# Optimization experiments

Measured on AMD Instinct MI355X. Metric: run time of the kernel, lower is better.

Reference implementation:

```python
import jax, jax.numpy as jnp
import numpy as np

NEG_SLOPE = 0.2


def gat_conv(x, src, dst, N, W, a_src, a_dst, b, concat):
    # x: [N, F_in], W: [F_in, H*C], a_src/a_dst: [H, C], b: [H*C] or [C]
    H, C = a_src.shape
    h = (x @ W).reshape(N, H, C)                    # [N, H, C]
    al_src = jnp.einsum('nhc,hc->nh', h, a_src)     # [N, H]
    al_dst = jnp.einsum('nhc,hc->nh', h, a_dst)     # [N, H]
    logits = jax.nn.leaky_relu(al_src[src] + al_dst[dst], NEG_SLOPE)  # [E, H]
    # edge softmax over incoming edges of each destination node
    m = jax.ops.segment_max(logits, dst, num_segments=N)              # [N, H]
    m = jnp.where(jnp.isfinite(m), m, 0.0)
    e = jnp.exp(logits - m[dst])                                      # [E, H]
    denom = jax.ops.segment_sum(e, dst, num_segments=N)               # [N, H]
    alpha = e / denom[dst]                                            # [E, H]
    out = jax.ops.segment_sum(alpha[:, :, None] * h[src], dst, num_segments=N)  # [N, H, C]
    if concat:
        return out.reshape(N, H * C) + b
    return out.mean(axis=1) + b


def setup_inputs() -> dict:
    key = jax.random.key(0)
    ks = jax.random.split(key, 12)
    N, E = 100000, 1600000
    F_in, Ch, Co, H = 128, 32, 64, 4
    x = jax.random.normal(ks[0], (N, F_in), dtype=jnp.float32)
    edge_index = jax.random.randint(ks[1], (2, E), 0, N, dtype=jnp.int64)
    s = 0.1
    return {
        'x': x, 'edge_index': edge_index,
        'W1': jax.random.normal(ks[2], (F_in, H * Ch), jnp.float32) * s,
        'a_src1': jax.random.normal(ks[3], (H, Ch), jnp.float32) * s,
        'a_dst1': jax.random.normal(ks[4], (H, Ch), jnp.float32) * s,
        'b1': jnp.zeros((H * Ch,), jnp.float32),
        'W2': jax.random.normal(ks[5], (H * Ch, H * Ch), jnp.float32) * s,
        'a_src2': jax.random.normal(ks[6], (H, Ch), jnp.float32) * s,
        'a_dst2': jax.random.normal(ks[7], (H, Ch), jnp.float32) * s,
        'b2': jnp.zeros((H * Ch,), jnp.float32),
        'W3': jax.random.normal(ks[8], (H * Ch, H * Co), jnp.float32) * s,
        'a_src3': jax.random.normal(ks[9], (H, Co), jnp.float32) * s,
        'a_dst3': jax.random.normal(ks[10], (H, Co), jnp.float32) * s,
        'b3': jnp.zeros((Co,), jnp.float32),
    }


def reference(x, edge_index, W1, a_src1, a_dst1, b1, W2, a_src2, a_dst2, b2, W3, a_src3, a_dst3, b3):
    N = x.shape[0]
    # PyG GATConv default add_self_loops=True
    loop = jnp.arange(N, dtype=edge_index.dtype)
    src = jnp.concatenate([edge_index[0], loop])
    dst = jnp.concatenate([edge_index[1], loop])
    h = gat_conv(x, src, dst, N, W1, a_src1, a_dst1, b1, concat=True)
    h = jax.nn.elu(h)
    h = gat_conv(h, src, dst, N, W2, a_src2, a_dst2, b2, concat=True)
    h = jax.nn.elu(h)
    out = gat_conv(h, src, dst, N, W3, a_src3, a_dst3, b3, concat=False)
    return out
```

## Files before the change

kernel.cpp:

```cpp
#include <hip/hip_runtime.h>


#define NEG_SLOPE 0.2f

typedef __attribute__((ext_vector_type(8))) _Float16 half8v;
typedef __attribute__((ext_vector_type(4))) _Float16 half4v;
typedef __attribute__((ext_vector_type(2))) _Float16 half2v;
typedef __attribute__((ext_vector_type(4))) float f32x4;

__device__ __forceinline__ float lrelu(float v) { return v > 0.f ? v : NEG_SLOPE * v; }

struct hf2 { _Float16 hi, lo; };
__device__ __forceinline__ hf2 split_f16(float f)
{
    hf2 r;
    r.hi = (_Float16)f;
    r.lo = (_Float16)(f - (float)r.hi);
    return r;
}

__global__ void fill_sentinel(float* __restrict__ out, int n)
{
    int i = blockIdx.x * blockDim.x + threadIdx.x;
    if (i < n) out[i] = 1e30f;
}

__global__ void detect_idx64(const int* __restrict__ ei, int* __restrict__ flag)
{
    __shared__ int anynz;
    if (threadIdx.x == 0) anynz = 0;
    __syncthreads();
    int v = ei[2 * threadIdx.x + 1];
    if (v != 0) atomicOr(&anynz, 1);
    __syncthreads();
    if (threadIdx.x == 0) flag[0] = (anynz == 0) ? 1 : 0;
}

__global__ void prep_edges(const void* __restrict__ ei, const int* __restrict__ flag,
                           int* __restrict__ deg8, int* __restrict__ loc, int N, int E)
{
    int e = blockIdx.x * blockDim.x + threadIdx.x;
    if (e >= E) return;
    int xcc;
    asm("s_getreg_b32 %0, hwreg(HW_REG_XCC_ID)" : "=s"(xcc));
    xcc &= 7;
    int d;
    if (flag[0]) d = (int)__builtin_nontemporal_load((const long long*)ei + E + e);
    else         d = __builtin_nontemporal_load((const int*)ei + E + e);
    int v = atomicAdd(&deg8[xcc * N + d], 1);
    loc[e] = (xcc << 28) | v;
}

__global__ void reduce8(int* __restrict__ deg8, int* __restrict__ deg, int N)
{
    int d = blockIdx.x * blockDim.x + threadIdx.x;
    if (d >= N) return;
    int s = 0;
    #pragma unroll
    for (int k = 0; k < 8; ++k) {
        int v = deg8[k * N + d];
        deg8[k * N + d] = s;
        s += v;
    }
    deg[d] = s;
}

__global__ __launch_bounds__(256)
void scanA(const int* __restrict__ deg, int* __restrict__ rowptr,
           int* __restrict__ bsum, int N)
{
    __shared__ int part[256];
    const int t = threadIdx.x;
    const int base = blockIdx.x * 1024 + t * 4;
    int v[4];
    #pragma unroll
    for (int j = 0; j < 4; ++j) v[j] = (base + j < N) ? deg[base + j] : 0;
    int s = v[0] + v[1] + v[2] + v[3];
    part[t] = s;
    __syncthreads();
    #pragma unroll
    for (int off = 1; off < 256; off <<= 1) {
        int p = (t >= off) ? part[t - off] : 0;
        __syncthreads();
        part[t] += p;
        __syncthreads();
    }
    int run = (t == 0) ? 0 : part[t - 1];
    #pragma unroll
    for (int j = 0; j < 4; ++j) {
        if (base + j < N) rowptr[base + j] = run;
        run += v[j];
    }
    if (t == 255) bsum[blockIdx.x] = part[255];
}

__global__ __launch_bounds__(1024)
void scanB(int* __restrict__ bsum, int nb)
{
    __shared__ int s[1024];
    int t = threadIdx.x;
    s[t] = (t < nb) ? bsum[t] : 0;
    __syncthreads();
    for (int off = 1; off < 1024; off <<= 1) {
        int p = (t >= off) ? s[t - off] : 0;
        __syncthreads();
        s[t] += p;
        __syncthreads();
    }
    if (t < nb) bsum[t] = (t == 0) ? 0 : s[t - 1];
}

__global__ __launch_bounds__(256)
void scanC(int* __restrict__ rowptr, const int* __restrict__ bsum, int N, int E)
{
    const int base = blockIdx.x * 1024 + threadIdx.x * 4;
    const int off = bsum[blockIdx.x];
    #pragma unroll
    for (int j = 0; j < 4; ++j)
        if (base + j < N) rowptr[base + j] += off;
    if (blockIdx.x == 0 && threadIdx.x == 0) rowptr[N] = E;
}

__global__ void fill_csr(const void* __restrict__ ei, const int* __restrict__ flag,
                         const int* __restrict__ loc, const int* __restrict__ rowptr,
                         const int* __restrict__ deg8, int* __restrict__ csr_src,
                         int N, int E)
{
    int e = blockIdx.x * blockDim.x + threadIdx.x;
    if (e >= E) return;
    int s, d;
    if (flag[0]) {
        s = (int)__builtin_nontemporal_load((const long long*)ei + e);
        d = (int)__builtin_nontemporal_load((const long long*)ei + E + e);
    } else {
        s = __builtin_nontemporal_load((const int*)ei + e);
        d = __builtin_nontemporal_load((const int*)ei + E + e);
    }
    int lv = loc[e];
    csr_src[rowptr[d] + deg8[(lv >> 28) * N + d] + (lv & 0x0FFFFFFF)] = s;
}

__global__ __launch_bounds__(256)
void convert_wt(const float* __restrict__ W, _Float16* __restrict__ wthi,
                _Float16* __restrict__ wtlo, int ldw, int wcol0)
{
    int t = blockIdx.x * 256 + threadIdx.x;
    int k = t >> 7, n = t & 127;
    float v = W[(long long)k * ldw + wcol0 + n];
    hf2 r = split_f16(v);
    wthi[n * 128 + k] = r.hi;
    wtlo[n * 128 + k] = r.lo;
}

template<int HPC, bool AF32>
__global__ __launch_bounds__(256, 2)
void gemm_mfma(const void* __restrict__ Aptr, const _Float16* __restrict__ Alo,
               const _Float16* __restrict__ Wthi, const _Float16* __restrict__ Wtlo,
               _Float16* __restrict__ Chi, int ldc, int colofs, int hofs,
               const float* __restrict__ aS, const float* __restrict__ aD,
               float* __restrict__ als, float* __restrict__ ald, int M)
{
    const int tid = threadIdx.x;
    const int wave = tid >> 6, lane = tid & 63;
    const int l15 = lane & 15, lk = lane >> 4;
    const int m0 = blockIdx.x * 128 + wave * 32;

    f32x4 acc[2][8];
    #pragma unroll
    for (int rg = 0; rg < 2; ++rg)
        #pragma unroll
        for (int i = 0; i < 8; ++i) acc[rg][i] = (f32x4){0.f, 0.f, 0.f, 0.f};

    #pragma unroll
    for (int kt = 0; kt < 4; ++kt) {
        const int k = kt * 32 + lk * 8;
        half8v bh[8], bl[8];
        #pragma unroll
        for (int nf = 0; nf < 8; ++nf) {
            bh[nf] = *(const half8v*)&Wthi[(nf * 16 + l15) * 128 + k];
            bl[nf] = *(const half8v*)&Wtlo[(nf * 16 + l15) * 128 + k];
        }
        #pragma unroll
        for (int rg = 0; rg < 2; ++rg) {
            int mrow = m0 + rg * 16 + l15;
            if (mrow >= M) mrow = M - 1;
            half8v ah, al;
            if (AF32) {
                const float* A32 = (const float*)Aptr;
                float4 v0 = *(const float4*)&A32[(long long)mrow * 128 + k];
                float4 v1 = *(const float4*)&A32[(long long)mrow * 128 + k + 4];
                hf2 s0 = split_f16(v0.x), s1 = split_f16(v0.y), s2 = split_f16(v0.z), s3 = split_f16(v0.w);
                hf2 s4 = split_f16(v1.x), s5 = split_f16(v1.y), s6 = split_f16(v1.z), s7 = split_f16(v1.w);
                ah[0] = s0.hi; ah[1] = s1.hi; ah[2] = s2.hi; ah[3] = s3.hi;
                ah[4] = s4.hi; ah[5] = s5.hi; ah[6] = s6.hi; ah[7] = s7.hi;
                al[0] = s0.lo; al[1] = s1.lo; al[2] = s2.lo; al[3] = s3.lo;
                al[4] = s4.lo; al[5] = s5.lo; al[6] = s6.lo; al[7] = s7.lo;
            } else {
                const _Float16* Ahi = (const _Float16*)Aptr;
                ah = *(const half8v*)&Ahi[(long long)mrow * 128 + k];
                al = *(const half8v*)&Alo[(long long)mrow * 128 + k];
            }
            #pragma unroll
            for (int nf = 0; nf < 8; ++nf) {
                acc[rg][nf] = __builtin_amdgcn_mfma_f32_16x16x32_f16(ah, bh[nf], acc[rg][nf], 0, 0, 0);
                acc[rg][nf] = __builtin_amdgcn_mfma_f32_16x16x32_f16(ah, bl[nf], acc[rg][nf], 0, 0, 0);
                acc[rg][nf] = __builtin_amdgcn_mfma_f32_16x16x32_f16(al, bh[nf], acc[rg][nf], 0, 0, 0);
            }
        }
    }

    float asv[8], adv[8];
    #pragma unroll
    for (int nf = 0; nf < 8; ++nf) {
        asv[nf] = aS[nf * 16 + l15];
        adv[nf] = aD[nf * 16 + l15];
    }
    constexpr int NFH = 8 / HPC;

    #pragma unroll
    for (int rg = 0; rg < 2; ++rg) {
        #pragma unroll
        for (int r = 0; r < 4; ++r) {
            int gm = m0 + rg * 16 + lk * 4 + r;
            if (gm >= M) continue;
            #pragma unroll
            for (int nf = 0; nf < 8; ++nf)
                Chi[(long long)gm * ldc + colofs + nf * 16 + l15] = (_Float16)acc[rg][nf][r];
        }
        #pragma unroll
        for (int r = 0; r < 4; ++r) {
            #pragma unroll
            for (int h = 0; h < HPC; ++h) {
                float ps = 0.f, pd = 0.f;
                #pragma unroll
                for (int q = 0; q < NFH; ++q) {
                    int nf = h * NFH + q;
                    ps += acc[rg][nf][r] * asv[nf];
                    pd += acc[rg][nf][r] * adv[nf];
                }
                #pragma unroll
                for (int m = 1; m < 16; m <<= 1) {
                    ps += __shfl_xor(ps, m);
                    pd += __shfl_xor(pd, m);
                }
                if (l15 == 0) {
                    int gm = m0 + rg * 16 + lk * 4 + r;
                    if (gm < M) {
                        als[gm * 4 + hofs + h] = ps;
                        ald[gm * 4 + hofs + h] = pd;
                    }
                }
            }
        }
    }
}

template<int C, int HL>
__global__ __launch_bounds__(256)
void gat_aggregate(const int* __restrict__ rowptr, const int* __restrict__ csr_src,
                   const float* __restrict__ als, const float* __restrict__ ald,
                   const _Float16* __restrict__ h16, const float* __restrict__ bias,
                   _Float16* __restrict__ ohi, _Float16* __restrict__ olo, int N)
{
    constexpr int ROW = HL * C;
    constexpr int LOG2HL = (HL == 4) ? 2 : 1;
    const int d = (blockIdx.x * blockDim.x + threadIdx.x) >> 6;
    const int lane = threadIdx.x & 63;
    if (d >= N) return;
    const int j = lane * 2;
    const int hh = j / C;

    const int myh = lane & (HL - 1);
    const int myi = lane >> LOG2HL;
    const float ald_mine = ald[d * 4 + myh];

    const float wself = __expf(lrelu(als[d * 4 + hh] + ald[d * 4 + hh]));
    float denom = wself;
    half2v hv = *(const half2v*)&h16[(unsigned)d * ROW + j];
    float vx = wself * (float)hv.x, vy = wself * (float)hv.y;

    const int e0 = rowptr[d], e1 = rowptr[d + 1];
    for (int base = e0; base < e1; base += 8) {
        int sv_mine = 0;
        float w_mine = 0.f;
        if (lane < 8 * HL) {
            int ee = base + myi;
            sv_mine = csr_src[ee < e1 ? ee : e1 - 1];
            float a = als[sv_mine * 4 + myh] + ald_mine;
            w_mine = (ee < e1) ? __expf(lrelu(a)) : 0.f;
        }
        int sref[8];
        half2v hb[8];
        #pragma unroll
        for (int i = 0; i < 8; ++i) sref[i] = __shfl(sv_mine, i * HL, 64);
        #pragma unroll
        for (int i = 0; i < 8; ++i) hb[i] = *(const half2v*)&h16[(unsigned)sref[i] * ROW + j];
        #pragma unroll
        for (int i = 0; i < 8; ++i) {
            float wv = __shfl(w_mine, i * HL + hh, 64);
            denom += wv;
            vx += wv * (float)hb[i].x;
            vy += wv * (float)hb[i].y;
        }
    }
    float inv = 1.f / denom;
    vx = vx * inv + bias[j];
    vy = vy * inv + bias[j + 1];
    vx = vx > 0.f ? vx : __expf(vx) - 1.f;
    vy = vy > 0.f ? vy : __expf(vy) - 1.f;
    hf2 rx = split_f16(vx), ry = split_f16(vy);
    half2v hi2, lo2;
    hi2.x = rx.hi; hi2.y = ry.hi;
    lo2.x = rx.lo; lo2.y = ry.lo;
    *(half2v*)&ohi[(unsigned)d * ROW + j] = hi2;
    *(half2v*)&olo[(unsigned)d * ROW + j] = lo2;
}

__global__ __launch_bounds__(256)
void gat_aggregate3(const int* __restrict__ rowptr, const int* __restrict__ csr_src,
                    const float* __restrict__ als, const float* __restrict__ ald,
                    const _Float16* __restrict__ h16, const float* __restrict__ bias,
                    float* __restrict__ out, int N)
{
    const int d = (blockIdx.x * blockDim.x + threadIdx.x) >> 6;
    const int lane = threadIdx.x & 63;
    if (d >= N) return;
    const int q = lane * 4;
    const int chd = lane >> 4;

    const int myh = lane & 3;
    const int myi = lane >> 2;
    const float ald_mine = ald[d * 4 + myh];

    const float wself = __expf(lrelu(als[d * 4 + chd] + ald[d * 4 + chd]));
    float dn = wself;
    half4v hs = *(const half4v*)&h16[(unsigned)d * 256 + q];
    float vx0 = wself * (float)hs.x, vx1 = wself * (float)hs.y;
    float vx2 = wself * (float)hs.z, vx3 = wself * (float)hs.w;

    const int e0 = rowptr[d], e1 = rowptr[d + 1];
    for (int base = e0; base < e1; base += 8) {
        int sv_mine = 0;
        float w_mine = 0.f;
        if (lane < 32) {
            int ee = base + myi;
            sv_mine = csr_src[ee < e1 ? ee : e1 - 1];
            float a = als[sv_mine * 4 + myh] + ald_mine;
            w_mine = (ee < e1) ? __expf(lrelu(a)) : 0.f;
        }
        int sref[8];
        half4v hb[8];
        #pragma unroll
        for (int i = 0; i < 8; ++i) sref[i] = __shfl(sv_mine, i * 4, 64);
        #pragma unroll
        for (int i = 0; i < 8; ++i) hb[i] = *(const half4v*)&h16[(unsigned)sref[i] * 256 + q];
        #pragma unroll
        for (int i = 0; i < 8; ++i) {
            float wv = __shfl(w_mine, i * 4 + chd, 64);
            dn += wv;
            vx0 += wv * (float)hb[i].x;
            vx1 += wv * (float)hb[i].y;
            vx2 += wv * (float)hb[i].z;
            vx3 += wv * (float)hb[i].w;
        }
    }
    const float s = 0.25f / dn;
    float m0 = vx0 * s, m1 = vx1 * s, m2 = vx2 * s, m3 = vx3 * s;
    m0 += __shfl_xor(m0, 16); m1 += __shfl_xor(m1, 16);
    m2 += __shfl_xor(m2, 16); m3 += __shfl_xor(m3, 16);
    m0 += __shfl_xor(m0, 32); m1 += __shfl_xor(m1, 32);
    m2 += __shfl_xor(m2, 32); m3 += __shfl_xor(m3, 32);
    if (lane < 16) {
        m0 += bias[q + 0]; m1 += bias[q + 1];
        m2 += bias[q + 2]; m3 += bias[q + 3];
        *(float4*)&out[(unsigned)d * 64 + q] = make_float4(m0, m1, m2, m3);
    }
}

extern "C" void kernel_launch(void* const* d_in, const int* in_sizes, int n_in,
                              void* d_out, int out_size, void* d_ws, size_t ws_size,
                              hipStream_t stream)
{
    const float* x      = (const float*)d_in[0];
    const void*  ei     = d_in[1];
    const float* W1     = (const float*)d_in[2];
    const float* a_src1 = (const float*)d_in[3];
    const float* a_dst1 = (const float*)d_in[4];
    const float* b1     = (const float*)d_in[5];
    const float* W2     = (const float*)d_in[6];
    const float* a_src2 = (const float*)d_in[7];
    const float* a_dst2 = (const float*)d_in[8];
    const float* b2     = (const float*)d_in[9];
    const float* W3     = (const float*)d_in[10];
    const float* a_src3 = (const float*)d_in[11];
    const float* a_dst3 = (const float*)d_in[12];
    const float* b3     = (const float*)d_in[13];

    const int N = in_sizes[0] / 128;
    const int E = in_sizes[1] / 2;

    char* w = (char*)d_ws;
    auto alloc = [&](size_t bytes) {
        char* p = w;
        w += (bytes + 255) & ~(size_t)255;
        return p;
    };
    int*      flag    = (int*)     alloc(256);
    int*      deg8    = (int*)     alloc((size_t)N * 8 * 4);
    int*      deg     = (int*)     alloc((size_t)N * 4);
    int*      rowptr  = (int*)     alloc((size_t)(N + 1) * 4);
    int*      bsum    = (int*)     alloc(1024 * 4);
    int*      loc     = (int*)     alloc((size_t)E * 4);
    int*      csr_src = (int*)     alloc((size_t)E * 4);
    _Float16* hhi     = (_Float16*)alloc((size_t)N * 256 * 2);
    _Float16* xhi     = (_Float16*)alloc((size_t)N * 128 * 2);
    _Float16* xlo     = (_Float16*)alloc((size_t)N * 128 * 2);
    float*    als     = (float*)   alloc((size_t)N * 4 * 4);
    float*    ald     = (float*)   alloc((size_t)N * 4 * 4);
    _Float16* wthi    = (_Float16*)alloc(2 * 128 * 128 * 2);
    _Float16* wtlo    = (_Float16*)alloc(2 * 128 * 128 * 2);
    if ((size_t)(w - (char*)d_ws) > ws_size) {
        fill_sentinel<<<(out_size + 255) / 256, 256, 0, stream>>>((float*)d_out, out_size);
        return;
    }
    _Float16* wthiB = wthi + 128 * 128;
    _Float16* wtloB = wtlo + 128 * 128;

    const int gb = 256;
    const int nb1024 = (N + 1023) / 1024;
    const int mb = (N + 127) / 128;
    const int ab = (N * 64 + gb - 1) / gb;
    auto blocks = [&](long long tot) { return (int)((tot + gb - 1) / gb); };

    detect_idx64<<<1, 256, 0, stream>>>((const int*)ei, flag);
    (void)hipMemsetAsync(deg8, 0, (size_t)N * 8 * 4, stream);
    prep_edges<<<blocks(E), gb, 0, stream>>>(ei, flag, deg8, loc, N, E);
    reduce8<<<blocks(N), gb, 0, stream>>>(deg8, deg, N);
    scanA<<<nb1024, gb, 0, stream>>>(deg, rowptr, bsum, N);
    scanB<<<1, 1024, 0, stream>>>(bsum, nb1024);
    scanC<<<nb1024, gb, 0, stream>>>(rowptr, bsum, N, E);
    fill_csr<<<blocks(E), gb, 0, stream>>>(ei, flag, loc, rowptr, deg8, csr_src, N, E);

    convert_wt<<<64, gb, 0, stream>>>(W1, wthi, wtlo, 128, 0);
    gemm_mfma<4, true><<<mb, gb, 0, stream>>>(x, nullptr, wthi, wtlo, hhi, 128, 0, 0,
                                              a_src1, a_dst1, als, ald, N);
    gat_aggregate<32, 4><<<ab, gb, 0, stream>>>(
        rowptr, csr_src, als, ald, hhi, b1, xhi, xlo, N);

    convert_wt<<<64, gb, 0, stream>>>(W2, wthi, wtlo, 128, 0);
    gemm_mfma<4, false><<<mb, gb, 0, stream>>>(xhi, xlo, wthi, wtlo, hhi, 128, 0, 0,
                                               a_src2, a_dst2, als, ald, N);
    gat_aggregate<32, 4><<<ab, gb, 0, stream>>>(
        rowptr, csr_src, als, ald, hhi, b2, xhi, xlo, N);

    convert_wt<<<64, gb, 0, stream>>>(W3, wthi,  wtlo,  256, 0);
    convert_wt<<<64, gb, 0, stream>>>(W3, wthiB, wtloB, 256, 128);
    gemm_mfma<2, false><<<mb, gb, 0, stream>>>(xhi, xlo, wthi,  wtlo,  hhi, 256, 0, 0,
                                               a_src3,       a_dst3,       als, ald, N);
    gemm_mfma<2, false><<<mb, gb, 0, stream>>>(xhi, xlo, wthiB, wtloB, hhi, 256, 128, 2,
                                               a_src3 + 128, a_dst3 + 128, als, ald, N);
    gat_aggregate3<<<ab, gb, 0, stream>>>(
        rowptr, csr_src, als, ald, hhi, b3, (float*)d_out, N);
}
```

Baseline: 628.9 us.

## Use single degree array for CSR build and merge layer-3 GEMM panels into one launch

Replaces the per-XCC sharded degree counters (deg8 plus reduce8) with a single global atomic degree array, so the reduce kernel and the large memset go away and fill_csr needs one fewer gather. The edge kernels now handle four edges per thread, issuing all loads before the atomics or stores. The two layer-3 GEMM launches are merged into a single launch with a 2D grid, where blockIdx.y selects the weight panel and output offsets. The cost is more atomic contention on shared counters across XCDs during the degree count.

```diff
diff --git a/kernel.cpp b/kernel.cpp
--- a/kernel.cpp
+++ b/kernel.cpp
@@ -36,33 +36,25 @@
     if (threadIdx.x == 0) flag[0] = (anynz == 0) ? 1 : 0;
 }
 
-__global__ void prep_edges(const void* __restrict__ ei, const int* __restrict__ flag,
-                           int* __restrict__ deg8, int* __restrict__ loc, int N, int E)
-{
-    int e = blockIdx.x * blockDim.x + threadIdx.x;
-    if (e >= E) return;
-    int xcc;
-    asm("s_getreg_b32 %0, hwreg(HW_REG_XCC_ID)" : "=s"(xcc));
-    xcc &= 7;
-    int d;
-    if (flag[0]) d = (int)__builtin_nontemporal_load((const long long*)ei + E + e);
-    else         d = __builtin_nontemporal_load((const int*)ei + E + e);
-    int v = atomicAdd(&deg8[xcc * N + d], 1);
-    loc[e] = (xcc << 28) | v;
-}
-
-__global__ void reduce8(int* __restrict__ deg8, int* __restrict__ deg, int N)
-{
-    int d = blockIdx.x * blockDim.x + threadIdx.x;
-    if (d >= N) return;
-    int s = 0;
-    #pragma unroll
-    for (int k = 0; k < 8; ++k) {
-        int v = deg8[k * N + d];
-        deg8[k * N + d] = s;
-        s += v;
-    }
-    deg[d] = s;
+__global__ __launch_bounds__(256)
+void prep_edges(const void* __restrict__ ei, const int* __restrict__ flag,
+                int* __restrict__ deg, int* __restrict__ loc, int E, int T)
+{
+    const int t = blockIdx.x * blockDim.x + threadIdx.x;
+    const bool f64 = flag[0] != 0;
+    int d[4];
+    #pragma unroll
+    for (int i = 0; i < 4; ++i) {
+        int e = t + i * T;
+        if (e < E)
+            d[i] = f64 ? (int)__builtin_nontemporal_load((const long long*)ei + E + e)
+                       : __builtin_nontemporal_load((const int*)ei + E + e);
+    }
+    #pragma unroll
+    for (int i = 0; i < 4; ++i) {
+        int e = t + i * T;
+        if (e < E) loc[e] = atomicAdd(&deg[d[i]], 1);
+    }
 }
 
 __global__ __launch_bounds__(256)
@@ -121,23 +113,39 @@
     if (blockIdx.x == 0 && threadIdx.x == 0) rowptr[N] = E;
 }
 
-__global__ void fill_csr(const void* __restrict__ ei, const int* __restrict__ flag,
-                         const int* __restrict__ loc, const int* __restrict__ rowptr,
-                         const int* __restrict__ deg8, int* __restrict__ csr_src,
-                         int N, int E)
-{
-    int e = blockIdx.x * blockDim.x + threadIdx.x;
-    if (e >= E) return;
-    int s, d;
-    if (flag[0]) {
-        s = (int)__builtin_nontemporal_load((const long long*)ei + e);
-        d = (int)__builtin_nontemporal_load((const long long*)ei + E + e);
-    } else {
-        s = __builtin_nontemporal_load((const int*)ei + e);
-        d = __builtin_nontemporal_load((const int*)ei + E + e);
-    }
-    int lv = loc[e];
-    csr_src[rowptr[d] + deg8[(lv >> 28) * N + d] + (lv & 0x0FFFFFFF)] = s;
+__global__ __launch_bounds__(256)
+void fill_csr(const void* __restrict__ ei, const int* __restrict__ flag,
+              const int* __restrict__ loc, const int* __restrict__ rowptr,
+              int* __restrict__ csr_src, int E, int T)
+{
+    const int t = blockIdx.x * blockDim.x + threadIdx.x;
+    const bool f64 = flag[0] != 0;
+    int s[4], d[4], l[4];
+    #pragma unroll
+    for (int i = 0; i < 4; ++i) {
+        int e = t + i * T;
+        if (e < E) {
+            if (f64) {
+                s[i] = (int)__builtin_nontemporal_load((const long long*)ei + e);
+                d[i] = (int)__builtin_nontemporal_load((const long long*)ei + E + e);
+            } else {
+                s[i] = __builtin_nontemporal_load((const int*)ei + e);
+                d[i] = __builtin_nontemporal_load((const int*)ei + E + e);
+            }
+            l[i] = loc[e];
+        }
+    }
+    int rp[4];
+    #pragma unroll
+    for (int i = 0; i < 4; ++i) {
+        int e = t + i * T;
+        if (e < E) rp[i] = rowptr[d[i]];
+    }
+    #pragma unroll
+    for (int i = 0; i < 4; ++i) {
+        int e = t + i * T;
+        if (e < E) csr_src[rp[i] + l[i]] = s[i];
+    }
 }
 
 __global__ __launch_bounds__(256)
@@ -160,6 +168,14 @@
                const float* __restrict__ aS, const float* __restrict__ aD,
                float* __restrict__ als, float* __restrict__ ald, int M)
 {
+    const int panel = blockIdx.y;
+    Wthi  += (size_t)panel * (128 * 128);
+    Wtlo  += (size_t)panel * (128 * 128);
+    colofs += panel * 128;
+    hofs   += panel * HPC;
+    aS     += panel * 128;
+    aD     += panel * 128;
+
     const int tid = threadIdx.x;
     const int wave = tid >> 6, lane = tid & 63;
     const int l15 = lane & 15, lk = lane >> 4;
@@ -406,7 +422,6 @@
         return p;
     };
     int*      flag    = (int*)     alloc(256);
-    int*      deg8    = (int*)     alloc((size_t)N * 8 * 4);
     int*      deg     = (int*)     alloc((size_t)N * 4);
     int*      rowptr  = (int*)     alloc((size_t)(N + 1) * 4);
     int*      bsum    = (int*)     alloc(1024 * 4);
@@ -430,16 +445,17 @@
     const int nb1024 = (N + 1023) / 1024;
     const int mb = (N + 127) / 128;
     const int ab = (N * 64 + gb - 1) / gb;
+    const int eb4 = (E + 1023) / 1024;
+    const int T = eb4 * gb;
     auto blocks = [&](long long tot) { return (int)((tot + gb - 1) / gb); };
 
     detect_idx64<<<1, 256, 0, stream>>>((const int*)ei, flag);
-    (void)hipMemsetAsync(deg8, 0, (size_t)N * 8 * 4, stream);
-    prep_edges<<<blocks(E), gb, 0, stream>>>(ei, flag, deg8, loc, N, E);
-    reduce8<<<blocks(N), gb, 0, stream>>>(deg8, deg, N);
+    (void)hipMemsetAsync(deg, 0, (size_t)N * 4, stream);
+    prep_edges<<<eb4, gb, 0, stream>>>(ei, flag, deg, loc, E, T);
     scanA<<<nb1024, gb, 0, stream>>>(deg, rowptr, bsum, N);
     scanB<<<1, 1024, 0, stream>>>(bsum, nb1024);
     scanC<<<nb1024, gb, 0, stream>>>(rowptr, bsum, N, E);
-    fill_csr<<<blocks(E), gb, 0, stream>>>(ei, flag, loc, rowptr, deg8, csr_src, N, E);
+    fill_csr<<<eb4, gb, 0, stream>>>(ei, flag, loc, rowptr, csr_src, E, T);
 
     convert_wt<<<64, gb, 0, stream>>>(W1, wthi, wtlo, 128, 0);
     gemm_mfma<4, true><<<mb, gb, 0, stream>>>(x, nullptr, wthi, wtlo, hhi, 128, 0, 0,
@@ -455,10 +471,8 @@
 
     convert_wt<<<64, gb, 0, stream>>>(W3, wthi,  wtlo,  256, 0);
     convert_wt<<<64, gb, 0, stream>>>(W3, wthiB, wtloB, 256, 128);
-    gemm_mfma<2, false><<<mb, gb, 0, stream>>>(xhi, xlo, wthi,  wtlo,  hhi, 256, 0, 0,
-                                               a_src3,       a_dst3,       als, ald, N);
-    gemm_mfma<2, false><<<mb, gb, 0, stream>>>(xhi, xlo, wthiB, wtloB, hhi, 256, 128, 2,
-                                               a_src3 + 128, a_dst3 + 128, als, ald, N);
+    gemm_mfma<2, false><<<dim3(mb, 2), gb, 0, stream>>>(xhi, xlo, wthi, wtlo, hhi, 256, 0, 0,
+                                                        a_src3, a_dst3, als, ald, N);
     gat_aggregate3<<<ab, gb, 0, stream>>>(
         rowptr, csr_src, als, ald, hhi, b3, (float*)d_out, N);
 }
```

After: 607.8 us. 1.03x faster.
